# Kernel optimization log

Measured on AMD Instinct MI355X. Metric: run time of the kernel, lower is better.

## Reference

```python
import jax, jax.numpy as jnp
import numpy as np

EMB = 1024
HEAD = 64
RANK = 8
LRA_SCL = 2.0
LORA = 1.0


def setup_inputs() -> dict:
    key = jax.random.key(0)
    ks = jax.random.split(key, 12)
    s = 1.0 / np.sqrt(EMB)
    sr = 1.0 / np.sqrt(RANK)
    inp = {
        "batEmb": jax.random.normal(ks[0], (8, 2048, EMB), dtype=jnp.float32),
        "tokMrk": jax.random.randint(ks[1], (8, 2048), 0, 2, dtype=jnp.int32),
        # base projections, nn.Linear weight layout [out, in]
        "Wq": jax.random.uniform(ks[2], (HEAD, EMB), jnp.float32, -s, s),
        "Wk": jax.random.uniform(ks[3], (HEAD, EMB), jnp.float32, -s, s),
        "Wv": jax.random.uniform(ks[4], (HEAD, EMB), jnp.float32, -s, s),
        # LoRA: A [rank, emb], B [head, rank]. (Original inits B to zero; we
        # randomize with small scale so the LoRA path is numerically exercised.)
        "Aq": jax.random.uniform(ks[5], (RANK, EMB), jnp.float32, -s, s),
        "Bq": jax.random.uniform(ks[6], (HEAD, RANK), jnp.float32, -sr, sr) * 0.02,
        "Ak": jax.random.uniform(ks[7], (RANK, EMB), jnp.float32, -s, s),
        "Bk": jax.random.uniform(ks[8], (HEAD, RANK), jnp.float32, -sr, sr) * 0.02,
        "Av": jax.random.uniform(ks[9], (RANK, EMB), jnp.float32, -s, s),
        "Bv": jax.random.uniform(ks[10], (HEAD, RANK), jnp.float32, -sr, sr) * 0.02,
    }
    return inp


def _proj(x, W, A, B):
    # base + LoRA low-rank delta (dropout = identity in eval)
    base = jnp.einsum('bse,he->bsh', x, W)
    lora = jnp.einsum('bsr,hr->bsh', jnp.einsum('bse,re->bsr', x, A), B)
    return base + lora * (LRA_SCL * LORA)


def reference(batEmb, tokMrk, Wq, Wk, Wv, Aq, Bq, Ak, Bk, Av, Bv):
    q = _proj(batEmb, Wq, Aq, Bq)  # [B,S,H]
    k = _proj(batEmb, Wk, Ak, Bk)
    v = _proj(batEmb, Wv, Av, Bv)
    w = jnp.einsum('bqh,bkh->bqk', q, k) * (HEAD ** -0.5)  # [B,S,S]
    mask = (tokMrk == 0)[:, None, :]  # [B,1,S] over key dim
    w = jnp.where(mask, -jnp.inf, w)
    w = jax.nn.softmax(w, axis=-1)
    w = jnp.nan_to_num(w, nan=0.0)
    return jnp.einsum('bqk,bkh->bqh', w, v)
```

## Files before the change

kernel.cpp:

```cpp
#include <hip/hip_runtime.h>
#include <hip/hip_bf16.h>
#include <stdint.h>

#define EMB 1024
#define NB 8
#define SEQ 2048
#define RANK 8
#define SPLIT 4

#define BM 64
#define BK 64
#define NSTG 16
#define BUFB 40960
#define NBUF 3

typedef __attribute__((ext_vector_type(8))) short bf16x8;
typedef __attribute__((ext_vector_type(4))) float f32x4;
typedef unsigned short u16;
typedef unsigned int u32;

__device__ __forceinline__ u16 f2bf(float f) {
  u32 u = __builtin_bit_cast(u32, f);
  u = (u + 0x7fffu + ((u >> 16) & 1u)) >> 16;
  return (u16)u;
}
__device__ __forceinline__ u32 pk2(float lo, float hi) {
  return (u32)f2bf(lo) | ((u32)f2bf(hi) << 16);
}
__device__ __forceinline__ u32 cvtpk(float lo, float hi) {
  __hip_bfloat162 h = __float22bfloat162_rn(make_float2(lo, hi));
  u32 u; __builtin_memcpy(&u, &h, 4); return u;
}
__device__ __forceinline__ void gll16(const void* g, void* l) {
  __builtin_amdgcn_global_load_lds(
      (const __attribute__((address_space(1))) unsigned int*)g,
      (__attribute__((address_space(3))) unsigned int*)l, 16, 0, 0);
}

#define PBAR()   asm volatile("s_barrier" ::: "memory")
#define WAITV(n) asm volatile("s_waitcnt vmcnt(" #n ")" ::: "memory")

__global__ __launch_bounds__(256) void fold_k(
    const float* __restrict__ Wq, const float* __restrict__ Wk, const float* __restrict__ Wv,
    const float* __restrict__ Aq, const float* __restrict__ Bq,
    const float* __restrict__ Ak, const float* __restrict__ Bk,
    const float* __restrict__ Av, const float* __restrict__ Bv,
    u16* __restrict__ weff) {
  int m = blockIdx.x;
  int mat = m >> 6, h = m & 63;
  const float* W = mat == 0 ? Wq : (mat == 1 ? Wk : Wv);
  const float* A = mat == 0 ? Aq : (mat == 1 ? Ak : Av);
  const float* B = mat == 0 ? Bq : (mat == 1 ? Bk : Bv);
  float bb[RANK];
#pragma unroll
  for (int r = 0; r < RANK; r++) bb[r] = 2.0f * B[h * RANK + r];
  int e = threadIdx.x * 4;
  float4 w4 = *(const float4*)(W + h * EMB + e);
  float a0 = w4.x, a1 = w4.y, a2 = w4.z, a3 = w4.w;
#pragma unroll
  for (int r = 0; r < RANK; r++) {
    float4 av = *(const float4*)(A + r * EMB + e);
    a0 += bb[r] * av.x; a1 += bb[r] * av.y; a2 += bb[r] * av.z; a3 += bb[r] * av.w;
  }
  u16* o = weff + (size_t)m * EMB + e;
  o[0] = f2bf(a0); o[1] = f2bf(a1); o[2] = f2bf(a2); o[3] = f2bf(a3);
}

__global__ __launch_bounds__(512) void proj_k(
    const float* __restrict__ X, const u16* __restrict__ weff,
    u16* __restrict__ qws, u16* __restrict__ kws, u16* __restrict__ vws) {
  extern __shared__ __align__(16) char smem[];

  int t = threadIdx.x;
  int w = t >> 6, l = t & 63;
  int rbase = blockIdx.x * BM;

  if (w >= 6) {
    int q = w - 6;
    int wkoff = ((l & 7) ^ (l >> 3)) * 8;
    int wc0 = l >> 3;
    int lr4 = l >> 4;
    int l15 = l & 15;

#define ISSUE(st, bufp) do {                                                   \
    _Pragma("unroll")                                                          \
    for (int i_ = 0; i_ < 8; i_++) {                                           \
      int rrel_ = q * 32 + i_ * 4 + lr4;                                       \
      int xo_ = 4 * (l15 ^ (rrel_ & 7));        \
      gll16(X + (size_t)(rbase + rrel_) * EMB + (st) * BK + xo_,               \
            (bufp) + q * 8192 + i_ * 1024);                                    \
    }                                                                          \
    _Pragma("unroll")                                                          \
    for (int i_ = 0; i_ < 12; i_++) { int wj_ = q * 12 + i_;                   \
      gll16(weff + (size_t)(wj_ * 8 + wc0) * EMB + (st) * BK + wkoff,          \
            (bufp) + 16384 + wj_ * 1024);                                      \
    } } while (0)

    ISSUE(0, smem);
    ISSUE(1, smem + BUFB);
    WAITV(20);
    for (int s = 0; s < NSTG; s++) {
      PBAR();
      if (s + 2 < NSTG) {
        ISSUE(s + 2, smem + ((s + 2) % NBUF) * BUFB);
        WAITV(20);
      } else if (s + 1 < NSTG) {
        WAITV(0);
      }
    }
#undef ISSUE
  } else {
    int l15 = l & 15, lh = l >> 4;
    f32x4 acc[4][2];
    f32x4 zero = {0.f, 0.f, 0.f, 0.f};
#pragma unroll
    for (int rt = 0; rt < 4; rt++)
#pragma unroll
      for (int ct = 0; ct < 2; ct++) acc[rt][ct] = zero;

    for (int s = 0; s < NSTG; s++) {
      PBAR();
      const char* bx = smem + (s % NBUF) * BUFB;
      const char* bw = bx + 16384;
#pragma unroll
      for (int j = 0; j < 2; j++) {
        bf16x8 a[4];
#pragma unroll
        for (int rt = 0; rt < 4; rt++) {
          int r = rt * 16 + l15;
          int sw = (r & 7) << 4;
          const char* base = bx + r * 256;
          f32x4 lo = *(const f32x4*)(base + ((j * 128 + lh * 32) ^ sw));
          f32x4 hi = *(const f32x4*)(base + ((j * 128 + lh * 32 + 16) ^ sw));
          union { bf16x8 v; u32 u[4]; } au;
          au.u[0] = cvtpk(lo.x, lo.y); au.u[1] = cvtpk(lo.z, lo.w);
          au.u[2] = cvtpk(hi.x, hi.y); au.u[3] = cvtpk(hi.z, hi.w);
          a[rt] = au.v;
        }
#pragma unroll
        for (int ct = 0; ct < 2; ct++) {
          int col = (w * 2 + ct) * 16 + l15;
          bf16x8 bf = *(const bf16x8*)(bw + col * 128 +
                                       ((j * 64 + lh * 16) ^ ((col & 7) << 4)));
#pragma unroll
          for (int rt = 0; rt < 4; rt++)
            acc[rt][ct] = __builtin_amdgcn_mfma_f32_16x16x32_bf16(a[rt], bf, acc[rt][ct], 0, 0, 0);
        }
      }
    }

#pragma unroll
    for (int rt = 0; rt < 4; rt++)
#pragma unroll
      for (int ct = 0; ct < 2; ct++) {
        int c = (w * 2 + ct) * 16 + l15;
#pragma unroll
        for (int r = 0; r < 4; r++) {
          int rr = rbase + rt * 16 + lh * 4 + r;
          float av = acc[rt][ct][r];
          if (c < 64) av *= 0.125f;
          u16 v = f2bf(av);
          if (c < 64) {
            qws[(size_t)rr * 64 + c] = v;
          } else if (c < 128) {
            kws[(size_t)rr * 64 + (c - 64)] = v;
          } else {
            int bb = rr >> 11, tok = rr & 2047;
            vws[((size_t)(bb * 64 + (c - 128))) * SEQ + tok] = v;
          }
        }
      }
  }
}

__global__ __launch_bounds__(256) void attn_k(
    const u16* __restrict__ qws, const u16* __restrict__ kws, const u16* __restrict__ vws,
    const int* __restrict__ mrk,
    float* __restrict__ po, float* __restrict__ pmp, float* __restrict__ plp) {
  __shared__ __align__(16) u16 ks[2 * 4096];
  __shared__ __align__(16) u16 vt[2 * 4096];
  __shared__ __align__(16) u16 ps[4 * 1024];

  int b = blockIdx.y;
  int z = blockIdx.z;
  int q0 = blockIdx.x * 64;
  int t = threadIdx.x;
  int w = t >> 6, l = t & 63;
  int l15 = l & 15, lh = l >> 4;

  int srow = t >> 3;
  int ssw = (((t & 7) << 4) ^ ((srow & 7) << 4)) >> 1;
  char* ksb = (char*)ks + w * 1024;
  char* vtb = (char*)vt + w * 1024;

  const u16* qp = qws + ((size_t)(b * SEQ + q0 + w * 16 + l15)) * 64 + lh * 8;
  bf16x8 qb0 = *(const bf16x8*)qp;
  bf16x8 qb1 = *(const bf16x8*)(qp + 32);

  f32x4 o[4];
  f32x4 zero = {0.f, 0.f, 0.f, 0.f};
#pragma unroll
  for (int ht = 0; ht < 4; ht++) o[ht] = zero;
  float mrow = -30000.0f, lrow = 0.f;

  int swz = (l15 & 7) << 4;
  int koffA = ((lh << 4) ^ swz) >> 1;
  int koffB = ((64 | (lh << 4)) ^ swz) >> 1;
  u16* psw = ps + w * 1024 + l15 * 64;

  const int NC = SEQ / 64 / SPLIT;
  int kk0 = z * (SEQ / SPLIT);

#define STAGE_KV(buf, kk)                                                          \
  do {                                                                             \
    gll16(kws + ((size_t)(b * SEQ + (kk) + srow)) * 64 + ssw,                      \
          ksb + (buf) * 8192);                                                     \
    gll16(kws + ((size_t)(b * SEQ + (kk) + srow + 32)) * 64 + ssw,                 \
          ksb + (buf) * 8192 + 4096);                                              \
    gll16(vws + ((size_t)(b * 64 + srow)) * SEQ + (kk) + ssw,                      \
          vtb + (buf) * 8192);                                                     \
    gll16(vws + ((size_t)(b * 64 + srow + 32)) * SEQ + (kk) + ssw,                 \
          vtb + (buf) * 8192 + 4096);                                              \
  } while (0)

  STAGE_KV(0, kk0);
  __syncthreads();

  int cur = 0;
  for (int kc = 0; kc < NC; kc++) {
    int kk = kk0 + kc * 64;
    if (kc + 1 < NC) STAGE_KV(cur ^ 1, kk + 64);

    int4 mi[4];
#pragma unroll
    for (int nt = 0; nt < 4; nt++)
      mi[nt] = *(const int4*)(mrk + b * SEQ + kk + nt * 16 + lh * 4);

    const u16* kb = ks + cur * 4096;
    f32x4 sa[4];
#pragma unroll
    for (int nt = 0; nt < 4; nt++) {
      const u16* kr = kb + (nt * 16 + l15) * 64;
      bf16x8 k0 = *(const bf16x8*)(kr + koffA);
      bf16x8 k1 = *(const bf16x8*)(kr + koffB);
      f32x4 s = zero;
      s = __builtin_amdgcn_mfma_f32_16x16x32_bf16(k0, qb0, s, 0, 0, 0);
      s = __builtin_amdgcn_mfma_f32_16x16x32_bf16(k1, qb1, s, 0, 0, 0);
      sa[nt] = s;
    }

    const u16* vbb = vt + cur * 4096;
    bf16x8 vb[4][2];
#pragma unroll
    for (int ht = 0; ht < 4; ht++) {
      const u16* vr = vbb + (ht * 16 + l15) * 64;
      vb[ht][0] = *(const bf16x8*)(vr + koffA);
      vb[ht][1] = *(const bf16x8*)(vr + koffB);
    }

#pragma unroll
    for (int nt = 0; nt < 4; nt++) {
      sa[nt][0] = mi[nt].x ? sa[nt][0] : -INFINITY;
      sa[nt][1] = mi[nt].y ? sa[nt][1] : -INFINITY;
      sa[nt][2] = mi[nt].z ? sa[nt][2] : -INFINITY;
      sa[nt][3] = mi[nt].w ? sa[nt][3] : -INFINITY;
    }
    float t0 = fmaxf(fmaxf(sa[0][0], sa[0][1]), fmaxf(sa[0][2], sa[0][3]));
    float t1 = fmaxf(fmaxf(sa[1][0], sa[1][1]), fmaxf(sa[1][2], sa[1][3]));
    float t2 = fmaxf(fmaxf(sa[2][0], sa[2][1]), fmaxf(sa[2][2], sa[2][3]));
    float t3 = fmaxf(fmaxf(sa[3][0], sa[3][1]), fmaxf(sa[3][2], sa[3][3]));
    float tm = fmaxf(fmaxf(t0, t1), fmaxf(t2, t3));
    tm = fmaxf(tm, __shfl_xor(tm, 16));
    tm = fmaxf(tm, __shfl_xor(tm, 32));

    if (!__all(tm <= mrow + 8.0f)) {
      float nm = fmaxf(mrow, tm);
      float alpha = __expf(mrow - nm);
      mrow = nm;
      lrow *= alpha;
      float a0 = __shfl(alpha, lh * 4 + 0);
      float a1 = __shfl(alpha, lh * 4 + 1);
      float a2 = __shfl(alpha, lh * 4 + 2);
      float a3 = __shfl(alpha, lh * 4 + 3);
#pragma unroll
      for (int ht = 0; ht < 4; ht++) {
        o[ht][0] *= a0; o[ht][1] *= a1; o[ht][2] *= a2; o[ht][3] *= a3;
      }
    }

    float ts = 0.f;
#pragma unroll
    for (int nt = 0; nt < 4; nt++) {
#pragma unroll
      for (int r = 0; r < 4; r++) {
        float p = __expf(sa[nt][r] - mrow);
        sa[nt][r] = p;
        ts += p;
      }
    }
    ts += __shfl_xor(ts, 16);
    ts += __shfl_xor(ts, 32);
    lrow += ts;

#pragma unroll
    for (int nt = 0; nt < 4; nt++) {
      u32 plo = pk2(sa[nt][0], sa[nt][1]);
      u32 phi = pk2(sa[nt][2], sa[nt][3]);
      *(uint2*)&psw[(((nt * 32 + lh * 8) ^ swz) >> 1)] = make_uint2(plo, phi);
    }
    bf16x8 ap0 = *(const bf16x8*)(psw + koffA);
    bf16x8 ap1 = *(const bf16x8*)(psw + koffB);

#pragma unroll
    for (int ht = 0; ht < 4; ht++) {
      o[ht] = __builtin_amdgcn_mfma_f32_16x16x32_bf16(ap0, vb[ht][0], o[ht], 0, 0, 0);
      o[ht] = __builtin_amdgcn_mfma_f32_16x16x32_bf16(ap1, vb[ht][1], o[ht], 0, 0, 0);
    }
    __syncthreads();
    cur ^= 1;
  }
#undef STAGE_KV

#pragma unroll
  for (int r = 0; r < 4; r++) {
    int rr = q0 + w * 16 + lh * 4 + r;
    float* pob = po + ((size_t)z * NB * SEQ + (size_t)b * SEQ + rr) * 64;
#pragma unroll
    for (int ht = 0; ht < 4; ht++) pob[ht * 16 + l15] = o[ht][r];
  }
  if (lh == 0) {
    int rr = q0 + w * 16 + l15;
    pmp[(size_t)z * NB * SEQ + (size_t)b * SEQ + rr] = mrow;
    plp[(size_t)z * NB * SEQ + (size_t)b * SEQ + rr] = lrow;
  }
}

__global__ __launch_bounds__(256) void merge_k(
    const float* __restrict__ po, const float* __restrict__ pmp,
    const float* __restrict__ plp, float* __restrict__ out) {
  int tid = threadIdx.x;
  int row = blockIdx.x * 32 + (tid >> 3);
  int c8 = (tid & 7) * 8;
  const int RT = NB * SEQ;

  float m[SPLIT], lv[SPLIT];
  float M = -INFINITY;
#pragma unroll
  for (int s = 0; s < SPLIT; s++) {
    m[s] = pmp[(size_t)s * RT + row];
    lv[s] = plp[(size_t)s * RT + row];
    M = fmaxf(M, m[s]);
  }
  float o8[8];
#pragma unroll
  for (int j = 0; j < 8; j++) o8[j] = 0.f;
  float L = 0.f;
  if (M != -INFINITY) {
#pragma unroll
    for (int s = 0; s < SPLIT; s++) {
      float ws = __expf(m[s] - M);
      L += ws * lv[s];
      const float* p = po + ((size_t)s * RT + row) * 64 + c8;
#pragma unroll
      for (int j = 0; j < 8; j++) o8[j] += ws * p[j];
    }
  }
  float inv = (L > 0.f) ? 1.0f / L : 0.f;
  float* op = out + (size_t)row * 64 + c8;
#pragma unroll
  for (int j = 0; j < 8; j++) op[j] = o8[j] * inv;
}

extern "C" void kernel_launch(void* const* d_in, const int* in_sizes, int n_in,
                              void* d_out, int out_size, void* d_ws, size_t ws_size,
                              hipStream_t stream) {
  const float* X   = (const float*)d_in[0];
  const int*   mrk = (const int*)d_in[1];
  const float* Wq  = (const float*)d_in[2];
  const float* Wk  = (const float*)d_in[3];
  const float* Wv  = (const float*)d_in[4];
  const float* Aq  = (const float*)d_in[5];
  const float* Bq  = (const float*)d_in[6];
  const float* Ak  = (const float*)d_in[7];
  const float* Bk  = (const float*)d_in[8];
  const float* Av  = (const float*)d_in[9];
  const float* Bv  = (const float*)d_in[10];

  u16* weff = (u16*)d_ws;
  u16* qws  = (u16*)((char*)d_ws + (512 << 10));
  u16* kws  = qws + (size_t)16384 * 64;
  u16* vws  = kws + (size_t)16384 * 64;
  float* po  = (float*)((char*)d_ws + ((size_t)6656 << 10));
  float* pmp = po + (size_t)SPLIT * 16384 * 64;
  float* plp = pmp + (size_t)SPLIT * 16384;

  (void)hipFuncSetAttribute((const void*)proj_k,
                            hipFuncAttributeMaxDynamicSharedMemorySize, NBUF * BUFB);

  fold_k<<<192, 256, 0, stream>>>(Wq, Wk, Wv, Aq, Bq, Ak, Bk, Av, Bv, weff);
  proj_k<<<256, 512, NBUF * BUFB, stream>>>(X, weff, qws, kws, vws);
  attn_k<<<dim3(32, 8, SPLIT), 256, 0, stream>>>(qws, kws, vws, mrk, po, pmp, plp);
  merge_k<<<512, 256, 0, stream>>>(po, pmp, plp, (float*)d_out);
}
```

Baseline: 61.67 us.

## Convert X to bf16 in producer warps and reshape projection warp layout

The projection kernel's producer warps now load X fp32 into registers, convert it to bf16 and write it to LDS, instead of DMAing fp32 into LDS and converting in every consumer warp. This halves the X LDS footprint and moves the conversion off the MFMA path. Consumers shrink from 6 to 3 warps, each computing 64 columns, with the pipeline unrolled three deep in registers. MFMA sections in both the projection and attention kernels are wrapped in s_setprio. Producer register pressure and hand-tuned waitcnt counts add risk.

Result: slower. 119.1 us (+93.1%).

```diff
diff --git a/kernel.cpp b/kernel.cpp
--- a/kernel.cpp
+++ b/kernel.cpp
@@ -11,7 +11,7 @@
 #define BM 64
 #define BK 64
 #define NSTG 16
-#define BUFB 40960
+#define BUFB 32768
 #define NBUF 3
 
 typedef __attribute__((ext_vector_type(8))) short bf16x8;
@@ -39,6 +39,8 @@
 
 #define PBAR()   asm volatile("s_barrier" ::: "memory")
 #define WAITV(n) asm volatile("s_waitcnt vmcnt(" #n ")" ::: "memory")
+#define WAITL()  asm volatile("s_waitcnt lgkmcnt(0)" ::: "memory")
+#define SB()     __builtin_amdgcn_sched_barrier(0)
 
 __global__ __launch_bounds__(256) void fold_k(
     const float* __restrict__ Wq, const float* __restrict__ Wk, const float* __restrict__ Wv,
@@ -66,7 +68,7 @@
   o[0] = f2bf(a0); o[1] = f2bf(a1); o[2] = f2bf(a2); o[3] = f2bf(a3);
 }
 
-__global__ __launch_bounds__(512) void proj_k(
+__global__ __launch_bounds__(320) void proj_k(
     const float* __restrict__ X, const u16* __restrict__ weff,
     u16* __restrict__ qws, u16* __restrict__ kws, u16* __restrict__ vws) {
   extern __shared__ __align__(16) char smem[];
@@ -75,85 +77,112 @@
   int w = t >> 6, l = t & 63;
   int rbase = blockIdx.x * BM;
 
-  if (w >= 6) {
-    int q = w - 6;
-    int wkoff = ((l & 7) ^ (l >> 3)) * 8;
+  if (w >= 3) {
+    int q = w - 3;
+    int p = q * 64 + l;
+    int pr = p >> 4;
+    int s16 = p & 15;
+    const float* xsrc = X + (size_t)(rbase + pr) * EMB + s16 * 4;
+    int xdoff = pr * 128 + ((s16 * 8) ^ ((pr & 7) << 4));
     int wc0 = l >> 3;
-    int lr4 = l >> 4;
-    int l15 = l & 15;
-
-#define ISSUE(st, bufp) do {                                                   \
-    _Pragma("unroll")                                                          \
-    for (int i_ = 0; i_ < 8; i_++) {                                           \
-      int rrel_ = q * 32 + i_ * 4 + lr4;                                       \
-      int xo_ = 4 * (l15 ^ (rrel_ & 7));        \
-      gll16(X + (size_t)(rbase + rrel_) * EMB + (st) * BK + xo_,               \
-            (bufp) + q * 8192 + i_ * 1024);                                    \
-    }                                                                          \
-    _Pragma("unroll")                                                          \
-    for (int i_ = 0; i_ < 12; i_++) { int wj_ = q * 12 + i_;                   \
-      gll16(weff + (size_t)(wj_ * 8 + wc0) * EMB + (st) * BK + wkoff,          \
-            (bufp) + 16384 + wj_ * 1024);                                      \
+    int wkoff = ((l & 7) ^ wc0) * 8;
+
+    float4 x0[8], x1[8], x2[8];
+
+#define ISSX(st, xr) do {                                                  \
+    _Pragma("unroll")                                                      \
+    for (int i_ = 0; i_ < 8; i_++)                                         \
+      xr[i_] = *(const float4*)(xsrc + (size_t)i_ * 8 * EMB + (st) * BK);  \
+  } while (0)
+
+#define WRITEX(bufp, xr) do {                                              \
+    _Pragma("unroll")                                                      \
+    for (int i_ = 0; i_ < 8; i_++) {                                       \
+      uint2 v_;                                                            \
+      v_.x = cvtpk(xr[i_].x, xr[i_].y);                                    \
+      v_.y = cvtpk(xr[i_].z, xr[i_].w);                                    \
+      *(uint2*)((bufp) + i_ * 1024 + xdoff) = v_;                          \
     } } while (0)
 
-    ISSUE(0, smem);
-    ISSUE(1, smem + BUFB);
+#define ISSW(st, bufp) do {                                                \
+    _Pragma("unroll")                                                      \
+    for (int i_ = 0; i_ < 12; i_++) { int wj_ = q * 12 + i_;               \
+      gll16(weff + (size_t)(wj_ * 8 + wc0) * EMB + (st) * BK + wkoff,      \
+            (bufp) + 8192 + wj_ * 1024);                                   \
+    } } while (0)
+
+    ISSX(0, x0); SB();
+    ISSX(1, x1); SB();
+    ISSW(0, smem); SB();
+    ISSX(2, x2); SB();
+    ISSW(1, smem + BUFB); SB();
+    WAITV(40);
+    WRITEX(smem, x0); WAITL();
     WAITV(20);
-    for (int s = 0; s < NSTG; s++) {
-      PBAR();
-      if (s + 2 < NSTG) {
-        ISSUE(s + 2, smem + ((s + 2) % NBUF) * BUFB);
-        WAITV(20);
-      } else if (s + 1 < NSTG) {
-        WAITV(0);
-      }
-    }
-#undef ISSUE
+    SB();
+
+#define PIT(s, LS, WS) do {                                                \
+    PBAR();                                                                \
+    if ((s) + 3 < NSTG) { ISSX((s) + 3, LS); SB(); }                       \
+    if ((s) + 2 < NSTG) { ISSW((s) + 2, smem + (((s) + 2) % NBUF) * BUFB); SB(); } \
+    WRITEX(smem + (((s) + 1) % NBUF) * BUFB, WS); WAITL();                 \
+    WAITV(20); SB();                                                       \
+  } while (0)
+
+    PIT(0, x0, x1);  PIT(1, x1, x2);  PIT(2, x2, x0);
+    PIT(3, x0, x1);  PIT(4, x1, x2);  PIT(5, x2, x0);
+    PIT(6, x0, x1);  PIT(7, x1, x2);  PIT(8, x2, x0);
+    PIT(9, x0, x1);  PIT(10, x1, x2); PIT(11, x2, x0);
+    PIT(12, x0, x1); PIT(13, x1, x2);
+    PBAR();
+    WAITV(12);
+    WRITEX(smem, x0); WAITL();
+    WAITV(0);
+    PBAR();
+#undef PIT
+#undef ISSX
+#undef WRITEX
+#undef ISSW
   } else {
     int l15 = l & 15, lh = l >> 4;
-    f32x4 acc[4][2];
+    f32x4 acc[4][4];
     f32x4 zero = {0.f, 0.f, 0.f, 0.f};
 #pragma unroll
     for (int rt = 0; rt < 4; rt++)
 #pragma unroll
-      for (int ct = 0; ct < 2; ct++) acc[rt][ct] = zero;
+      for (int ct = 0; ct < 4; ct++) acc[rt][ct] = zero;
 
     for (int s = 0; s < NSTG; s++) {
       PBAR();
       const char* bx = smem + (s % NBUF) * BUFB;
-      const char* bw = bx + 16384;
+      const char* bw = bx + 8192;
 #pragma unroll
       for (int j = 0; j < 2; j++) {
         bf16x8 a[4];
 #pragma unroll
         for (int rt = 0; rt < 4; rt++) {
           int r = rt * 16 + l15;
-          int sw = (r & 7) << 4;
-          const char* base = bx + r * 256;
-          f32x4 lo = *(const f32x4*)(base + ((j * 128 + lh * 32) ^ sw));
-          f32x4 hi = *(const f32x4*)(base + ((j * 128 + lh * 32 + 16) ^ sw));
-          union { bf16x8 v; u32 u[4]; } au;
-          au.u[0] = cvtpk(lo.x, lo.y); au.u[1] = cvtpk(lo.z, lo.w);
-          au.u[2] = cvtpk(hi.x, hi.y); au.u[3] = cvtpk(hi.z, hi.w);
-          a[rt] = au.v;
+          a[rt] = *(const bf16x8*)(bx + r * 128 + ((j * 64 + lh * 16) ^ ((r & 7) << 4)));
         }
-#pragma unroll
-        for (int ct = 0; ct < 2; ct++) {
-          int col = (w * 2 + ct) * 16 + l15;
+        __builtin_amdgcn_s_setprio(1);
+#pragma unroll
+        for (int ct = 0; ct < 4; ct++) {
+          int col = w * 64 + ct * 16 + l15;
           bf16x8 bf = *(const bf16x8*)(bw + col * 128 +
                                        ((j * 64 + lh * 16) ^ ((col & 7) << 4)));
 #pragma unroll
           for (int rt = 0; rt < 4; rt++)
             acc[rt][ct] = __builtin_amdgcn_mfma_f32_16x16x32_bf16(a[rt], bf, acc[rt][ct], 0, 0, 0);
         }
+        __builtin_amdgcn_s_setprio(0);
       }
     }
 
 #pragma unroll
     for (int rt = 0; rt < 4; rt++)
 #pragma unroll
-      for (int ct = 0; ct < 2; ct++) {
-        int c = (w * 2 + ct) * 16 + l15;
+      for (int ct = 0; ct < 4; ct++) {
+        int c = w * 64 + ct * 16 + l15;
 #pragma unroll
         for (int r = 0; r < 4; r++) {
           int rr = rbase + rt * 16 + lh * 4 + r;
@@ -238,6 +267,7 @@
 
     const u16* kb = ks + cur * 4096;
     f32x4 sa[4];
+    __builtin_amdgcn_s_setprio(1);
 #pragma unroll
     for (int nt = 0; nt < 4; nt++) {
       const u16* kr = kb + (nt * 16 + l15) * 64;
@@ -248,6 +278,7 @@
       s = __builtin_amdgcn_mfma_f32_16x16x32_bf16(k1, qb1, s, 0, 0, 0);
       sa[nt] = s;
     }
+    __builtin_amdgcn_s_setprio(0);
 
     const u16* vbb = vt + cur * 4096;
     bf16x8 vb[4][2];
@@ -311,11 +342,13 @@
     bf16x8 ap0 = *(const bf16x8*)(psw + koffA);
     bf16x8 ap1 = *(const bf16x8*)(psw + koffB);
 
+    __builtin_amdgcn_s_setprio(1);
 #pragma unroll
     for (int ht = 0; ht < 4; ht++) {
       o[ht] = __builtin_amdgcn_mfma_f32_16x16x32_bf16(ap0, vb[ht][0], o[ht], 0, 0, 0);
       o[ht] = __builtin_amdgcn_mfma_f32_16x16x32_bf16(ap1, vb[ht][1], o[ht], 0, 0, 0);
     }
+    __builtin_amdgcn_s_setprio(0);
     __syncthreads();
     cur ^= 1;
   }
@@ -398,7 +431,7 @@
                             hipFuncAttributeMaxDynamicSharedMemorySize, NBUF * BUFB);
 
   fold_k<<<192, 256, 0, stream>>>(Wq, Wk, Wv, Aq, Bq, Ak, Bk, Av, Bv, weff);
-  proj_k<<<256, 512, NBUF * BUFB, stream>>>(X, weff, qws, kws, vws);
+  proj_k<<<256, 320, NBUF * BUFB, stream>>>(X, weff, qws, kws, vws);
   attn_k<<<dim3(32, 8, SPLIT), 256, 0, stream>>>(qws, kws, vws, mrk, po, pmp, plp);
   merge_k<<<512, 256, 0, stream>>>(po, pmp, plp, (float*)d_out);
 }
```
